# Kernel optimization log

Hardware: AMD Instinct MI355X
Metric: run time of the kernel (lower is better)

The kernel has to match this reference:

```python
import jax, jax.numpy as jnp
import numpy as np

NEG_BIG = -9.0e15  # matches -9000000000000000.0 in the torch source


def setup_inputs() -> dict:
    key = jax.random.key(0)
    k1, k2 = jax.random.split(key)
    N, D, L = 8192, 128, 2
    features = jax.random.normal(k1, (N, D), dtype=jnp.float32)
    adj_lst = jax.random.randint(k2, (L, N, N), 0, 2, dtype=jnp.int32)
    return {"features": features, "adj_lst": adj_lst}


def reference(features, adj_lst):
    # features: [N, D] float; adj_lst: [L, N, N] int (0/1)
    n_node = features.shape[0]
    for i in range(adj_lst.shape[0]):  # small fixed number of propagation steps
        adj = adj_lst[i]
        mask = adj > 0
        # raw_weight = ones -> masked logits are 1.0 on edges, -9e15 elsewhere
        logits = jnp.where(mask, jnp.float32(1.0), jnp.float32(NEG_BIG))
        attention = jax.nn.softmax(logits, axis=1)          # [N, N] row-stochastic
        prop_fea = attention @ features                     # [N, D] neighbor mean
        adj_num = jnp.sum(adj, axis=1)                      # degree per node
        adj_mask = (adj_num > 0).astype(features.dtype)[:, None]  # [N, 1]
        features = adj_mask * prop_fea + (1.0 - adj_mask) * features
    return features
```

## Files before the change

kernel.cpp:

```cpp
#include <hip/hip_runtime.h>
#include <hip/hip_bf16.h>

typedef __bf16 bf16x8 __attribute__((ext_vector_type(8)));
typedef float f32x4 __attribute__((ext_vector_type(4)));
typedef int int4v __attribute__((ext_vector_type(4)));
typedef unsigned int uint4v __attribute__((ext_vector_type(4)));
typedef unsigned short u16x8 __attribute__((ext_vector_type(8)));

#define N_NODES 8192
#define D_FEAT 128

__global__ __launch_bounds__(256) void pack_bpk_kernel(
    const int* __restrict__ adj, unsigned long long* __restrict__ bits64,
    int* __restrict__ deg, const float* __restrict__ fsrc,
    unsigned short* __restrict__ Bpk) {
  const int bx = blockIdx.x;
  const int t = threadIdx.x;

  if (bx >= N_NODES) {
    const int W = (bx - N_NODES) * 256 + t;
    const int kk = W >> 9;
    const int nt = (W >> 6) & 7;
    const int l = W & 63;
    const int d = nt * 16 + (l & 15);
    const int p0 = kk * 32 + (l >> 4) * 8;
    const int n0 = (p0 >> 8) * 256 + ((p0 >> 3) & 7) * 32 + ((p0 >> 6) & 3);
    u16x8 pk;
#pragma unroll
    for (int e = 0; e < 8; ++e) {
      __bf16 v = (__bf16)fsrc[(long)(n0 + 4 * e) * D_FEAT + d];
      pk[e] = __builtin_bit_cast(unsigned short, v);
    }
    *(u16x8*)(Bpk + (long)W * 8) = pk;
    return;
  }

  const int row = bx;
  const int w = t >> 6;
  const int lane = t & 63;
  const int4v* p = (const int4v*)(adj + ((long)row << 13));
  int4v v[8];
#pragma unroll
  for (int j = 0; j < 8; ++j) v[j] = p[j * 256 + t];

  unsigned long long* brow = bits64 + ((long)row << 7);
  int cnt = 0;
#pragma unroll
  for (int j = 0; j < 8; ++j) {
    unsigned long long b0 = __ballot(v[j][0] != 0);
    unsigned long long b1 = __ballot(v[j][1] != 0);
    unsigned long long b2 = __ballot(v[j][2] != 0);
    unsigned long long b3 = __ballot(v[j][3] != 0);
    cnt += __popcll(b0) + __popcll(b1) + __popcll(b2) + __popcll(b3);
    unsigned long long bsel = b0;
    if (lane == 1) bsel = b1;
    if (lane == 2) bsel = b2;
    if (lane == 3) bsel = b3;
    if (lane < 4) brow[16 * j + 4 * w + lane] = bsel;
  }
  __shared__ int red[4];
  if (lane == 0) red[w] = cnt;
  __syncthreads();
  if (t == 0) deg[row] = red[0] + red[1] + red[2] + red[3];
}

__global__ __launch_bounds__(256) void bpk_build_kernel(
    const float* __restrict__ src, unsigned short* __restrict__ Bpk) {
  const int W = blockIdx.x * 256 + threadIdx.x;
  const int kk = W >> 9;
  const int nt = (W >> 6) & 7;
  const int l = W & 63;
  const int d = nt * 16 + (l & 15);
  const int p0 = kk * 32 + (l >> 4) * 8;
  const int n0 = (p0 >> 8) * 256 + ((p0 >> 3) & 7) * 32 + ((p0 >> 6) & 3);
  u16x8 pk;
#pragma unroll
  for (int e = 0; e < 8; ++e) {
    __bf16 v = (__bf16)src[(long)(n0 + 4 * e) * D_FEAT + d];
    pk[e] = __builtin_bit_cast(unsigned short, v);
  }
  *(u16x8*)(Bpk + (long)W * 8) = pk;
}

__device__ __forceinline__ bf16x8 unpack_byte(unsigned dword, int sh) {
  unsigned P = ((dword >> sh) & 0xFFu) * 0x8001u;
  uint4v c;
  c[0] = (P & 0x10001u) * 0x3F80u;
  c[1] = ((P >> 2) & 0x10001u) * 0x3F80u;
  c[2] = ((P >> 4) & 0x10001u) * 0x3F80u;
  c[3] = ((P >> 6) & 0x10001u) * 0x3F80u;
  return __builtin_bit_cast(bf16x8, c);
}

__device__ __forceinline__ void layer_body(
    int rowblk, int nthalf,
    const unsigned* __restrict__ bits, const int* __restrict__ deg,
    const unsigned short* __restrict__ Bpk,
    const float* __restrict__ fin, float* __restrict__ fout,
    f32x4 (*red)[64][4]) {
  const int tid = threadIdx.x;
  const int lane = tid & 63;
  const int w = tid >> 6;
  const int ntl = w & 3;
  const int kh = w >> 2;
  const int lr = lane & 15;
  const int kc = lane >> 4;
  const int sh = kc * 8;
  const int m0 = rowblk * 64;
  const int nt = nthalf * 4 + ntl;

  const uint4v* ap0 =
      (const uint4v*)(bits + ((long)(m0 + lr) << 8)) + kh * 32;
  const bf16x8* bp = (const bf16x8*)Bpk + nt * 64 + lane + (kh << 16);

  f32x4 acc[4];
#pragma unroll
  for (int mt = 0; mt < 4; ++mt) acc[mt] = {0.f, 0.f, 0.f, 0.f};

  for (int kg = 0; kg < 32; ++kg) {
    uint4v a0 = ap0[kg];
    uint4v a1 = ap0[kg + 1024];
    uint4v a2 = ap0[kg + 2048];
    uint4v a3 = ap0[kg + 3072];
#pragma unroll
    for (int b = 0; b < 4; ++b) {
      bf16x8 bv = *bp;
      bp += 512;
      acc[0] = __builtin_amdgcn_mfma_f32_16x16x32_bf16(unpack_byte(a0[b], sh),
                                                       bv, acc[0], 0, 0, 0);
      acc[1] = __builtin_amdgcn_mfma_f32_16x16x32_bf16(unpack_byte(a1[b], sh),
                                                       bv, acc[1], 0, 0, 0);
      acc[2] = __builtin_amdgcn_mfma_f32_16x16x32_bf16(unpack_byte(a2[b], sh),
                                                       bv, acc[2], 0, 0, 0);
      acc[3] = __builtin_amdgcn_mfma_f32_16x16x32_bf16(unpack_byte(a3[b], sh),
                                                       bv, acc[3], 0, 0, 0);
    }
  }

  if (kh) {
#pragma unroll
    for (int mt = 0; mt < 4; ++mt) red[ntl][lane][mt] = acc[mt];
  }
  __syncthreads();
  if (kh) return;
#pragma unroll
  for (int mt = 0; mt < 4; ++mt) acc[mt] += red[ntl][lane][mt];

#pragma unroll
  for (int mt = 0; mt < 4; ++mt) {
#pragma unroll
    for (int j = 0; j < 4; ++j) {
      const int row = m0 + mt * 16 + kc * 4 + j;
      const int dg = deg[row];
      const long off = (long)row * D_FEAT + nt * 16 + lr;
      fout[off] = dg > 0 ? acc[mt][j] * (1.0f / (float)dg) : fin[off];
    }
  }
}

__global__ __launch_bounds__(512, 2) void layer1_pack2_kernel(
    const int* __restrict__ adj2, unsigned long long* __restrict__ bits64_l2,
    int* __restrict__ deg_l2, const unsigned* __restrict__ bits_l1,
    const int* __restrict__ deg_l1, const unsigned short* __restrict__ Bpk,
    const float* __restrict__ fin, float* __restrict__ fout) {
  __shared__ __align__(16) f32x4 red[4][64][4];
  const int bx = blockIdx.x;
  if (bx < 256) {
    layer_body(bx >> 1, bx & 1, bits_l1, deg_l1, Bpk, fin, fout, red);
    return;
  }
  const int t = threadIdx.x;
  const int half = t >> 8;
  const int tt = t & 255;
  const int w4 = tt >> 6;
  const int lane = t & 63;
  const int row = (bx - 256) * 2 + half;
  const int4v* p = (const int4v*)(adj2 + ((long)row << 13));
  int4v v[8];
#pragma unroll
  for (int j = 0; j < 8; ++j) v[j] = p[j * 256 + tt];

  unsigned long long* brow = bits64_l2 + ((long)row << 7);
  int cnt = 0;
#pragma unroll
  for (int j = 0; j < 8; ++j) {
    unsigned long long b0 = __ballot(v[j][0] != 0);
    unsigned long long b1 = __ballot(v[j][1] != 0);
    unsigned long long b2 = __ballot(v[j][2] != 0);
    unsigned long long b3 = __ballot(v[j][3] != 0);
    cnt += __popcll(b0) + __popcll(b1) + __popcll(b2) + __popcll(b3);
    unsigned long long bsel = b0;
    if (lane == 1) bsel = b1;
    if (lane == 2) bsel = b2;
    if (lane == 3) bsel = b3;
    if (lane < 4) brow[16 * j + 4 * w4 + lane] = bsel;
  }
  __shared__ int red2[2][4];
  if (lane == 0) red2[half][w4] = cnt;
  __syncthreads();
  if (tt == 0) deg_l2[row] = red2[half][0] + red2[half][1] +
                             red2[half][2] + red2[half][3];
}

__global__ __launch_bounds__(512, 2) void layer_std_kernel(
    const unsigned* __restrict__ bits, const int* __restrict__ deg,
    const unsigned short* __restrict__ Bpk,
    const float* __restrict__ fin, float* __restrict__ fout) {
  __shared__ __align__(16) f32x4 red[4][64][4];
  const int bx = blockIdx.x;
  layer_body(bx >> 1, bx & 1, bits, deg, Bpk, fin, fout, red);
}

__global__ __launch_bounds__(256) void transpose_cast_kernel(
    const float* __restrict__ src, unsigned short* __restrict__ dst) {
  __shared__ float tile[64][129];
  const int t = threadIdx.x;
  const int nbase = blockIdx.x * 64;
#pragma unroll
  for (int i = 0; i < 32; ++i) {
    int idx = t + i * 256;
    int nl = idx >> 7;
    int d = idx & 127;
    tile[nl][d] = src[(long)(nbase + nl) * D_FEAT + d];
  }
  __syncthreads();
#pragma unroll
  for (int i = 0; i < 32; ++i) {
    int idx = t + i * 256;
    int d = idx >> 6;
    int nl = idx & 63;
    __bf16 b = (__bf16)tile[nl][d];
    dst[(long)d * N_NODES + nbase + nl] = __builtin_bit_cast(unsigned short, b);
  }
}

__global__ __launch_bounds__(512) void layer_kernel_direct(
    const int* __restrict__ adj, const unsigned short* __restrict__ BT,
    const float* __restrict__ fin, float* __restrict__ fout) {
  const int tid = threadIdx.x;
  const int lane = tid & 63;
  const int w = tid >> 6;
  const int m0 = blockIdx.x * 32 + (w >> 2) * 16;
  const int n0 = (w & 3) * 32;
  const int lr = lane & 15;
  const int kc = lane >> 4;

  const int4v* ap = (const int4v*)(adj + (long)(m0 + lr) * N_NODES + kc * 8);
  const bf16x8* bp0 = (const bf16x8*)(BT + (long)(n0 + lr) * N_NODES + kc * 8);
  const bf16x8* bp1 = (const bf16x8*)(BT + (long)(n0 + 16 + lr) * N_NODES + kc * 8);

  f32x4 acc0 = {0.f, 0.f, 0.f, 0.f};
  f32x4 acc1 = {0.f, 0.f, 0.f, 0.f};
  int degv = 0;

#pragma unroll 4
  for (int k = 0; k < N_NODES; k += 32) {
    int4v alo = ap[0];
    int4v ahi = ap[1];
    bf16x8 b0 = bp0[0];
    bf16x8 b1 = bp1[0];
    ap += 8; bp0 += 4; bp1 += 4;
    unsigned short u[8];
    u[0] = alo[0] ? 0x3F80 : 0;
    u[1] = alo[1] ? 0x3F80 : 0;
    u[2] = alo[2] ? 0x3F80 : 0;
    u[3] = alo[3] ? 0x3F80 : 0;
    u[4] = ahi[0] ? 0x3F80 : 0;
    u[5] = ahi[1] ? 0x3F80 : 0;
    u[6] = ahi[2] ? 0x3F80 : 0;
    u[7] = ahi[3] ? 0x3F80 : 0;
    degv += alo[0] + alo[1] + alo[2] + alo[3] + ahi[0] + ahi[1] + ahi[2] + ahi[3];
    bf16x8 a;
    memcpy(&a, u, 16);
    acc0 = __builtin_amdgcn_mfma_f32_16x16x32_bf16(a, b0, acc0, 0, 0, 0);
    acc1 = __builtin_amdgcn_mfma_f32_16x16x32_bf16(a, b1, acc1, 0, 0, 0);
  }

  degv += __shfl_xor(degv, 16);
  degv += __shfl_xor(degv, 32);
  int dgv[4];
#pragma unroll
  for (int j = 0; j < 4; ++j) dgv[j] = __shfl(degv, kc * 4 + j);

#pragma unroll
  for (int t = 0; t < 2; ++t) {
    const f32x4 acc = t ? acc1 : acc0;
    const int col = n0 + t * 16 + lr;
#pragma unroll
    for (int j = 0; j < 4; ++j) {
      const long off = (long)(m0 + kc * 4 + j) * D_FEAT + col;
      fout[off] = dgv[j] > 0 ? acc[j] * (1.0f / (float)dgv[j]) : fin[off];
    }
  }
}

extern "C" void kernel_launch(void* const* d_in, const int* in_sizes, int n_in,
                              void* d_out, int out_size, void* d_ws, size_t ws_size,
                              hipStream_t stream) {
  const float* features = (const float*)d_in[0];
  const int* adj = (const int*)d_in[1];
  float* out = (float*)d_out;
  const long NN = (long)N_NODES * N_NODES;

  const size_t BITS_BYTES = 2ul * N_NODES * 128 * 8;
  const size_t BPK_BYTES = (size_t)D_FEAT * N_NODES * 2;
  const size_t NEED = BITS_BYTES + 65536 + BPK_BYTES;

  if (ws_size >= NEED) {
    unsigned long long* bits64 = (unsigned long long*)d_ws;
    int* degw = (int*)((char*)d_ws + BITS_BYTES);
    unsigned short* Bpk = (unsigned short*)((char*)d_ws + BITS_BYTES + 65536);
    const unsigned* bits32 = (const unsigned*)d_ws;

    pack_bpk_kernel<<<N_NODES + 512, 256, 0, stream>>>(
        adj, bits64, degw, features, Bpk);
    layer1_pack2_kernel<<<256 + N_NODES / 2, 512, 0, stream>>>(
        adj + NN, bits64 + (size_t)N_NODES * 128, degw + N_NODES,
        bits32, degw, Bpk, features, out);
    bpk_build_kernel<<<512, 256, 0, stream>>>(out, Bpk);
    layer_std_kernel<<<256, 512, 0, stream>>>(
        bits32 + (size_t)N_NODES * 256, degw + N_NODES, Bpk, out, out);
  } else {
    unsigned short* BTw = (unsigned short*)d_ws;
    transpose_cast_kernel<<<N_NODES / 64, 256, 0, stream>>>(features, BTw);
    layer_kernel_direct<<<N_NODES / 32, 512, 0, stream>>>(adj, BTw, features, out);
    transpose_cast_kernel<<<N_NODES / 64, 256, 0, stream>>>(out, BTw);
    layer_kernel_direct<<<N_NODES / 32, 512, 0, stream>>>(adj + NN, BTw, out, out);
  }
}
```

Before: 177.3 us.

## Switch layer GEMM to 32x32x16 MFMA with 4-way K split and unfused packing

```diff
diff --git a/kernel.cpp b/kernel.cpp
--- a/kernel.cpp
+++ b/kernel.cpp
@@ -3,6 +3,7 @@
 
 typedef __bf16 bf16x8 __attribute__((ext_vector_type(8)));
 typedef float f32x4 __attribute__((ext_vector_type(4)));
+typedef float f32x16 __attribute__((ext_vector_type(16)));
 typedef int int4v __attribute__((ext_vector_type(4)));
 typedef unsigned int uint4v __attribute__((ext_vector_type(4)));
 typedef unsigned short u16x8 __attribute__((ext_vector_type(8)));
@@ -10,32 +11,47 @@
 #define N_NODES 8192
 #define D_FEAT 128
 
-__global__ __launch_bounds__(256) void pack_bpk_kernel(
+__device__ __forceinline__ bf16x8 unpack_byte(unsigned dword, int sh) {
+  unsigned P = ((dword >> sh) & 0xFFu) * 0x8001u;
+  uint4v c;
+  c[0] = (P & 0x10001u) * 0x3F80u;
+  c[1] = ((P >> 2) & 0x10001u) * 0x3F80u;
+  c[2] = ((P >> 4) & 0x10001u) * 0x3F80u;
+  c[3] = ((P >> 6) & 0x10001u) * 0x3F80u;
+  return __builtin_bit_cast(bf16x8, c);
+}
+
+__device__ __forceinline__ void bpk32_store(const float* __restrict__ src,
+                                            unsigned short* __restrict__ Bpk,
+                                            int W) {
+  const int kk = W >> 8;
+  const int ng = (W >> 6) & 3;
+  const int l = W & 63;
+  const int d = ng * 32 + (l & 31);
+  const int p0 = kk * 16 + (l >> 5) * 8;
+  const int n0 = (p0 >> 8) * 256 + ((p0 >> 3) & 7) * 32 + ((p0 >> 6) & 3);
+  u16x8 pk;
+#pragma unroll
+  for (int e = 0; e < 8; ++e) {
+    __bf16 v = (__bf16)src[(long)(n0 + 4 * e) * D_FEAT + d];
+    pk[e] = __builtin_bit_cast(unsigned short, v);
+  }
+  *(u16x8*)(Bpk + (long)W * 8) = pk;
+}
+
+__global__ __launch_bounds__(256) void pack_all_kernel(
     const int* __restrict__ adj, unsigned long long* __restrict__ bits64,
     int* __restrict__ deg, const float* __restrict__ fsrc,
     unsigned short* __restrict__ Bpk) {
   const int bx = blockIdx.x;
   const int t = threadIdx.x;
 
-  if (bx >= N_NODES) {
-    const int W = (bx - N_NODES) * 256 + t;
-    const int kk = W >> 9;
-    const int nt = (W >> 6) & 7;
-    const int l = W & 63;
-    const int d = nt * 16 + (l & 15);
-    const int p0 = kk * 32 + (l >> 4) * 8;
-    const int n0 = (p0 >> 8) * 256 + ((p0 >> 3) & 7) * 32 + ((p0 >> 6) & 3);
-    u16x8 pk;
-#pragma unroll
-    for (int e = 0; e < 8; ++e) {
-      __bf16 v = (__bf16)fsrc[(long)(n0 + 4 * e) * D_FEAT + d];
-      pk[e] = __builtin_bit_cast(unsigned short, v);
-    }
-    *(u16x8*)(Bpk + (long)W * 8) = pk;
+  if (bx < 512) {
+    bpk32_store(fsrc, Bpk, bx * 256 + t);
     return;
   }
 
-  const int row = bx;
+  const int row = bx - 512;
   const int w = t >> 6;
   const int lane = t & 63;
   const int4v* p = (const int4v*)(adj + ((long)row << 13));
@@ -64,151 +80,103 @@
   if (t == 0) deg[row] = red[0] + red[1] + red[2] + red[3];
 }
 
-__global__ __launch_bounds__(256) void bpk_build_kernel(
+__global__ __launch_bounds__(256) void bpk_build32_kernel(
     const float* __restrict__ src, unsigned short* __restrict__ Bpk) {
-  const int W = blockIdx.x * 256 + threadIdx.x;
-  const int kk = W >> 9;
-  const int nt = (W >> 6) & 7;
-  const int l = W & 63;
-  const int d = nt * 16 + (l & 15);
-  const int p0 = kk * 32 + (l >> 4) * 8;
-  const int n0 = (p0 >> 8) * 256 + ((p0 >> 3) & 7) * 32 + ((p0 >> 6) & 3);
-  u16x8 pk;
-#pragma unroll
-  for (int e = 0; e < 8; ++e) {
-    __bf16 v = (__bf16)src[(long)(n0 + 4 * e) * D_FEAT + d];
-    pk[e] = __builtin_bit_cast(unsigned short, v);
-  }
-  *(u16x8*)(Bpk + (long)W * 8) = pk;
-}
-
-__device__ __forceinline__ bf16x8 unpack_byte(unsigned dword, int sh) {
-  unsigned P = ((dword >> sh) & 0xFFu) * 0x8001u;
-  uint4v c;
-  c[0] = (P & 0x10001u) * 0x3F80u;
-  c[1] = ((P >> 2) & 0x10001u) * 0x3F80u;
-  c[2] = ((P >> 4) & 0x10001u) * 0x3F80u;
-  c[3] = ((P >> 6) & 0x10001u) * 0x3F80u;
-  return __builtin_bit_cast(bf16x8, c);
-}
-
-__device__ __forceinline__ void layer_body(
+  bpk32_store(src, Bpk, blockIdx.x * 256 + threadIdx.x);
+}
+
+__device__ __forceinline__ void layer_body32(
     int rowblk, int nthalf,
     const unsigned* __restrict__ bits, const int* __restrict__ deg,
     const unsigned short* __restrict__ Bpk,
-    const float* __restrict__ fin, float* __restrict__ fout,
-    f32x4 (*red)[64][4]) {
+    const float* fin, float* fout,
+    f32x4 (*red)[2][2][4][64]) {
   const int tid = threadIdx.x;
   const int lane = tid & 63;
   const int w = tid >> 6;
-  const int ntl = w & 3;
-  const int kh = w >> 2;
-  const int lr = lane & 15;
-  const int kc = lane >> 4;
-  const int sh = kc * 8;
+  const int ntl = w & 1;
+  const int kh = w >> 1;
+  const int l31 = lane & 31;
+  const int lh = lane >> 5;
   const int m0 = rowblk * 64;
-  const int nt = nthalf * 4 + ntl;
-
-  const uint4v* ap0 =
-      (const uint4v*)(bits + ((long)(m0 + lr) << 8)) + kh * 32;
-  const bf16x8* bp = (const bf16x8*)Bpk + nt * 64 + lane + (kh << 16);
-
-  f32x4 acc[4];
-#pragma unroll
-  for (int mt = 0; mt < 4; ++mt) acc[mt] = {0.f, 0.f, 0.f, 0.f};
-
-  for (int kg = 0; kg < 32; ++kg) {
+  const int ng = nthalf * 2 + ntl;
+  const int shA = lh * 8;
+  const int shB = shA + 16;
+
+  const uint4v* ap0 = (const uint4v*)(bits + ((long)(m0 + l31) << 8)) + kh * 16;
+  const uint4v* ap1 =
+      (const uint4v*)(bits + ((long)(m0 + 32 + l31) << 8)) + kh * 16;
+  const bf16x8* bp = (const bf16x8*)Bpk + ((long)kh << 15) + ng * 64 + lane;
+
+  f32x16 acc0 = {0.f, 0.f, 0.f, 0.f, 0.f, 0.f, 0.f, 0.f,
+                 0.f, 0.f, 0.f, 0.f, 0.f, 0.f, 0.f, 0.f};
+  f32x16 acc1 = {0.f, 0.f, 0.f, 0.f, 0.f, 0.f, 0.f, 0.f,
+                 0.f, 0.f, 0.f, 0.f, 0.f, 0.f, 0.f, 0.f};
+
+#pragma unroll 2
+  for (int kg = 0; kg < 16; ++kg) {
     uint4v a0 = ap0[kg];
-    uint4v a1 = ap0[kg + 1024];
-    uint4v a2 = ap0[kg + 2048];
-    uint4v a3 = ap0[kg + 3072];
-#pragma unroll
-    for (int b = 0; b < 4; ++b) {
+    uint4v a1 = ap1[kg];
+#pragma unroll
+    for (int s = 0; s < 8; ++s) {
       bf16x8 bv = *bp;
-      bp += 512;
-      acc[0] = __builtin_amdgcn_mfma_f32_16x16x32_bf16(unpack_byte(a0[b], sh),
-                                                       bv, acc[0], 0, 0, 0);
-      acc[1] = __builtin_amdgcn_mfma_f32_16x16x32_bf16(unpack_byte(a1[b], sh),
-                                                       bv, acc[1], 0, 0, 0);
-      acc[2] = __builtin_amdgcn_mfma_f32_16x16x32_bf16(unpack_byte(a2[b], sh),
-                                                       bv, acc[2], 0, 0, 0);
-      acc[3] = __builtin_amdgcn_mfma_f32_16x16x32_bf16(unpack_byte(a3[b], sh),
-                                                       bv, acc[3], 0, 0, 0);
+      bp += 256;
+      const int sh = (s & 1) ? shB : shA;
+      acc0 = __builtin_amdgcn_mfma_f32_32x32x16_bf16(
+          unpack_byte(a0[s >> 1], sh), bv, acc0, 0, 0, 0);
+      acc1 = __builtin_amdgcn_mfma_f32_32x32x16_bf16(
+          unpack_byte(a1[s >> 1], sh), bv, acc1, 0, 0, 0);
     }
   }
 
   if (kh) {
-#pragma unroll
-    for (int mt = 0; mt < 4; ++mt) red[ntl][lane][mt] = acc[mt];
+#define STORE_CHUNK(c)                                                       \
+  red[kh - 1][ntl][0][c][lane] = __builtin_shufflevector(                    \
+      acc0, acc0, 4 * (c), 4 * (c) + 1, 4 * (c) + 2, 4 * (c) + 3);           \
+  red[kh - 1][ntl][1][c][lane] = __builtin_shufflevector(                    \
+      acc1, acc1, 4 * (c), 4 * (c) + 1, 4 * (c) + 2, 4 * (c) + 3);
+    STORE_CHUNK(0)
+    STORE_CHUNK(1)
+    STORE_CHUNK(2)
+    STORE_CHUNK(3)
+#undef STORE_CHUNK
   }
   __syncthreads();
   if (kh) return;
-#pragma unroll
-  for (int mt = 0; mt < 4; ++mt) acc[mt] += red[ntl][lane][mt];
-
-#pragma unroll
-  for (int mt = 0; mt < 4; ++mt) {
-#pragma unroll
-    for (int j = 0; j < 4; ++j) {
-      const int row = m0 + mt * 16 + kc * 4 + j;
+
+#pragma unroll
+  for (int q = 0; q < 3; ++q) {
+#pragma unroll
+    for (int c = 0; c < 4; ++c) {
+      f32x4 r0 = red[q][ntl][0][c][lane];
+      f32x4 r1 = red[q][ntl][1][c][lane];
+#pragma unroll
+      for (int k = 0; k < 4; ++k) {
+        acc0[4 * c + k] += r0[k];
+        acc1[4 * c + k] += r1[k];
+      }
+    }
+  }
+
+#pragma unroll
+  for (int mt = 0; mt < 2; ++mt) {
+#pragma unroll
+    for (int r = 0; r < 16; ++r) {
+      const int row = m0 + mt * 32 + (r & 3) + 8 * (r >> 2) + 4 * lh;
       const int dg = deg[row];
-      const long off = (long)row * D_FEAT + nt * 16 + lr;
-      fout[off] = dg > 0 ? acc[mt][j] * (1.0f / (float)dg) : fin[off];
+      const float a = mt ? acc1[r] : acc0[r];
+      const long off = (long)row * D_FEAT + ng * 32 + l31;
+      fout[off] = dg > 0 ? a * (1.0f / (float)dg) : fin[off];
     }
   }
 }
 
-__global__ __launch_bounds__(512, 2) void layer1_pack2_kernel(
-    const int* __restrict__ adj2, unsigned long long* __restrict__ bits64_l2,
-    int* __restrict__ deg_l2, const unsigned* __restrict__ bits_l1,
-    const int* __restrict__ deg_l1, const unsigned short* __restrict__ Bpk,
-    const float* __restrict__ fin, float* __restrict__ fout) {
-  __shared__ __align__(16) f32x4 red[4][64][4];
-  const int bx = blockIdx.x;
-  if (bx < 256) {
-    layer_body(bx >> 1, bx & 1, bits_l1, deg_l1, Bpk, fin, fout, red);
-    return;
-  }
-  const int t = threadIdx.x;
-  const int half = t >> 8;
-  const int tt = t & 255;
-  const int w4 = tt >> 6;
-  const int lane = t & 63;
-  const int row = (bx - 256) * 2 + half;
-  const int4v* p = (const int4v*)(adj2 + ((long)row << 13));
-  int4v v[8];
-#pragma unroll
-  for (int j = 0; j < 8; ++j) v[j] = p[j * 256 + tt];
-
-  unsigned long long* brow = bits64_l2 + ((long)row << 7);
-  int cnt = 0;
-#pragma unroll
-  for (int j = 0; j < 8; ++j) {
-    unsigned long long b0 = __ballot(v[j][0] != 0);
-    unsigned long long b1 = __ballot(v[j][1] != 0);
-    unsigned long long b2 = __ballot(v[j][2] != 0);
-    unsigned long long b3 = __ballot(v[j][3] != 0);
-    cnt += __popcll(b0) + __popcll(b1) + __popcll(b2) + __popcll(b3);
-    unsigned long long bsel = b0;
-    if (lane == 1) bsel = b1;
-    if (lane == 2) bsel = b2;
-    if (lane == 3) bsel = b3;
-    if (lane < 4) brow[16 * j + 4 * w4 + lane] = bsel;
-  }
-  __shared__ int red2[2][4];
-  if (lane == 0) red2[half][w4] = cnt;
-  __syncthreads();
-  if (tt == 0) deg_l2[row] = red2[half][0] + red2[half][1] +
-                             red2[half][2] + red2[half][3];
-}
-
-__global__ __launch_bounds__(512, 2) void layer_std_kernel(
+__global__ __launch_bounds__(512, 2) void layer32_kernel(
     const unsigned* __restrict__ bits, const int* __restrict__ deg,
-    const unsigned short* __restrict__ Bpk,
-    const float* __restrict__ fin, float* __restrict__ fout) {
-  __shared__ __align__(16) f32x4 red[4][64][4];
-  const int bx = blockIdx.x;
-  layer_body(bx >> 1, bx & 1, bits, deg, Bpk, fin, fout, red);
+    const unsigned short* __restrict__ Bpk, const float* fin, float* fout) {
+  __shared__ __align__(16) f32x4 red[3][2][2][4][64];
+  layer_body32(blockIdx.x >> 1, blockIdx.x & 1, bits, deg, Bpk, fin, fout,
+               red);
 }
 
 __global__ __launch_bounds__(256) void transpose_cast_kernel(
@@ -247,7 +215,8 @@
 
   const int4v* ap = (const int4v*)(adj + (long)(m0 + lr) * N_NODES + kc * 8);
   const bf16x8* bp0 = (const bf16x8*)(BT + (long)(n0 + lr) * N_NODES + kc * 8);
-  const bf16x8* bp1 = (const bf16x8*)(BT + (long)(n0 + 16 + lr) * N_NODES + kc * 8);
+  const bf16x8* bp1 =
+      (const bf16x8*)(BT + (long)(n0 + 16 + lr) * N_NODES + kc * 8);
 
   f32x4 acc0 = {0.f, 0.f, 0.f, 0.f};
   f32x4 acc1 = {0.f, 0.f, 0.f, 0.f};
@@ -259,7 +228,9 @@
     int4v ahi = ap[1];
     bf16x8 b0 = bp0[0];
     bf16x8 b1 = bp1[0];
-    ap += 8; bp0 += 4; bp1 += 4;
+    ap += 8;
+    bp0 += 4;
+    bp1 += 4;
     unsigned short u[8];
     u[0] = alo[0] ? 0x3F80 : 0;
     u[1] = alo[1] ? 0x3F80 : 0;
@@ -269,7 +240,8 @@
     u[5] = ahi[1] ? 0x3F80 : 0;
     u[6] = ahi[2] ? 0x3F80 : 0;
     u[7] = ahi[3] ? 0x3F80 : 0;
-    degv += alo[0] + alo[1] + alo[2] + alo[3] + ahi[0] + ahi[1] + ahi[2] + ahi[3];
+    degv += alo[0] + alo[1] + alo[2] + alo[3] + ahi[0] + ahi[1] + ahi[2] +
+            ahi[3];
     bf16x8 a;
     memcpy(&a, u, 16);
     acc0 = __builtin_amdgcn_mfma_f32_16x16x32_bf16(a, b0, acc0, 0, 0, 0);
@@ -295,8 +267,8 @@
 }
 
 extern "C" void kernel_launch(void* const* d_in, const int* in_sizes, int n_in,
-                              void* d_out, int out_size, void* d_ws, size_t ws_size,
-                              hipStream_t stream) {
+                              void* d_out, int out_size, void* d_ws,
+                              size_t ws_size, hipStream_t stream) {
   const float* features = (const float*)d_in[0];
   const int* adj = (const int*)d_in[1];
   float* out = (float*)d_out;
@@ -312,19 +284,19 @@
     unsigned short* Bpk = (unsigned short*)((char*)d_ws + BITS_BYTES + 65536);
     const unsigned* bits32 = (const unsigned*)d_ws;
 
-    pack_bpk_kernel<<<N_NODES + 512, 256, 0, stream>>>(
-        adj, bits64, degw, features, Bpk);
-    layer1_pack2_kernel<<<256 + N_NODES / 2, 512, 0, stream>>>(
-        adj + NN, bits64 + (size_t)N_NODES * 128, degw + N_NODES,
-        bits32, degw, Bpk, features, out);
-    bpk_build_kernel<<<512, 256, 0, stream>>>(out, Bpk);
-    layer_std_kernel<<<256, 512, 0, stream>>>(
-        bits32 + (size_t)N_NODES * 256, degw + N_NODES, Bpk, out, out);
+    pack_all_kernel<<<2 * N_NODES + 512, 256, 0, stream>>>(adj, bits64, degw,
+                                                           features, Bpk);
+    layer32_kernel<<<256, 512, 0, stream>>>(bits32, degw, Bpk, features, out);
+    bpk_build32_kernel<<<512, 256, 0, stream>>>(out, Bpk);
+    layer32_kernel<<<256, 512, 0, stream>>>(bits32 + (size_t)N_NODES * 256,
+                                            degw + N_NODES, Bpk, out, out);
   } else {
     unsigned short* BTw = (unsigned short*)d_ws;
     transpose_cast_kernel<<<N_NODES / 64, 256, 0, stream>>>(features, BTw);
-    layer_kernel_direct<<<N_NODES / 32, 512, 0, stream>>>(adj, BTw, features, out);
+    layer_kernel_direct<<<N_NODES / 32, 512, 0, stream>>>(adj, BTw, features,
+                                                          out);
     transpose_cast_kernel<<<N_NODES / 64, 256, 0, stream>>>(out, BTw);
-    layer_kernel_direct<<<N_NODES / 32, 512, 0, stream>>>(adj + NN, BTw, out, out);
-  }
-}
+    layer_kernel_direct<<<N_NODES / 32, 512, 0, stream>>>(adj + NN, BTw, out,
+                                                          out);
+  }
+}
```

After: 175.5 us. No clear change (-1.0%).
